# Kernel tuning notes

Measured on AMD Instinct MI355X. Metric: run time of the kernel, lower is better.

Reference implementation:

```python
import jax, jax.numpy as jnp
import numpy as np

B, N, D, H = 8, 1024, 512, 512  # batch, nodes/graph, input dim, hidden/output dim
NEG_SLOPE = 0.2


def _gatv2_layer(x, src, dst, Wl, bl, Wr, br, a, bias, nseg):
    """PyG GATv2Conv (heads=1, add_self_loops=False, eval mode -> no dropout).
    message j->i: alpha_ij = softmax_i( a . leaky_relu(xl[j] + xr[i]) ); out[i] = sum_j alpha_ij * xl[j] + bias
    """
    xl = x @ Wl + bl              # [nseg, H] source transform
    xr = x @ Wr + br              # [nseg, H] target transform
    e = jax.nn.leaky_relu(xl[src] + xr[dst], NEG_SLOPE) @ a  # [E] raw scores
    m = jax.lax.stop_gradient(jax.ops.segment_max(e, dst, num_segments=nseg))
    ex = jnp.exp(e - m[dst])
    s = jax.ops.segment_sum(ex, dst, num_segments=nseg)
    alpha = ex / s[dst]                                       # segment softmax over incoming edges
    out = jax.ops.segment_sum(alpha[:, None] * xl[src], dst, num_segments=nseg)
    return out + bias


def setup_inputs() -> dict:
    key = jax.random.key(0)
    rng = np.random.RandomState(0)
    # random per-graph adjacency, avg degree ~16; block-diagonal edge extraction
    adj_np = (rng.rand(B, N, N) < (16.0 / N))
    srcs, dsts = [], []
    for b in range(B):  # matches torch.nonzero(big_adj).t(): row=src, col=dst
        r, c = np.nonzero(adj_np[b])
        srcs.append(r + b * N)
        dsts.append(c + b * N)
    edge_index = jnp.asarray(np.stack([np.concatenate(srcs), np.concatenate(dsts)]).astype(np.int32))

    ks = jax.random.split(key, 32)
    def lin(k, fi, fo):
        return (jax.random.normal(k, (fi, fo), jnp.float32) / np.sqrt(fi)).astype(jnp.float32)
    inp = {
        "batch_graph": jax.random.normal(ks[0], (B, N, D), jnp.float32),
        "adj": jnp.asarray(adj_np.astype(np.float32)),
        "edge_index": edge_index,
    }
    dims = [(D, H), (H, H), (H, H)]
    for i, (fi, fo) in enumerate(dims, start=1):
        k = jax.random.split(ks[i], 6)
        inp[f"Wl{i}"] = lin(k[0], fi, fo)
        inp[f"bl{i}"] = jnp.zeros((fo,), jnp.float32)
        inp[f"Wr{i}"] = lin(k[1], fi, fo)
        inp[f"br{i}"] = jnp.zeros((fo,), jnp.float32)
        inp[f"a{i}"] = (jax.random.normal(k[2], (fo,), jnp.float32) / np.sqrt(fo)).astype(jnp.float32)
        inp[f"bias{i}"] = jnp.zeros((fo,), jnp.float32)
    return inp


def reference(batch_graph, adj, edge_index,
              Wl1, bl1, Wr1, br1, a1, bias1,
              Wl2, bl2, Wr2, br2, a2, bias2,
              Wl3, bl3, Wr3, br3, a3, bias3):
    b, n, d = batch_graph.shape
    nseg = b * n
    x = batch_graph.reshape(nseg, d)
    src, dst = edge_index[0], edge_index[1]
    x = _gatv2_layer(x, src, dst, Wl1, bl1, Wr1, br1, a1, bias1, nseg)  # graph_norm = Identity
    x = _gatv2_layer(x, src, dst, Wl2, bl2, Wr2, br2, a2, bias2, nseg)
    x = _gatv2_layer(x, src, dst, Wl3, bl3, Wr3, br3, a3, bias3, nseg)
    return x.reshape(b, n, -1)
```

## Files before the change

### kernel.cpp

```cpp
#include <hip/hip_runtime.h>
#include <math.h>

#define MTOT 8192
#define HD   512
#define NEG  0.2f

typedef __attribute__((ext_vector_type(8))) short bf16x8;
typedef __attribute__((ext_vector_type(4))) float floatx4;

__device__ inline unsigned short f2bf(float f) {
    unsigned int u = __float_as_uint(f);
    unsigned int r = (u + 0x7FFFu + ((u >> 16) & 1u)) >> 16;
    return (unsigned short)r;
}
__device__ inline float bf2f(unsigned short h) {
    return __uint_as_float(((unsigned int)h) << 16);
}


__global__ void count_deg(const int* __restrict__ dst, int* __restrict__ deg, int E) {
    int i = blockIdx.x * 256 + threadIdx.x;
    if (i < E) atomicAdd(&deg[dst[i]], 1);
}

__global__ __launch_bounds__(1024) void scan_offsets(const int* __restrict__ deg,
                                                     int* __restrict__ offs,
                                                     int* __restrict__ cursor) {
    __shared__ int part[1024];
    int tid = threadIdx.x;
    int base = tid * 8;
    int v[8]; int s = 0;
    #pragma unroll
    for (int i = 0; i < 8; ++i) { v[i] = deg[base + i]; s += v[i]; }
    part[tid] = s;
    __syncthreads();
    for (int off = 1; off < 1024; off <<= 1) {
        int t = (tid >= off) ? part[tid - off] : 0;
        __syncthreads();
        part[tid] += t;
        __syncthreads();
    }
    int run = (tid == 0) ? 0 : part[tid - 1];
    #pragma unroll
    for (int i = 0; i < 8; ++i) {
        offs[base + i] = run;
        cursor[base + i] = run;
        run += v[i];
    }
    if (tid == 1023) offs[MTOT] = run;
}

__global__ void scatter_edges(const int* __restrict__ src, const int* __restrict__ dst,
                              int* __restrict__ cursor, int* __restrict__ csr_src, int E) {
    int i = blockIdx.x * 256 + threadIdx.x;
    if (i < E) {
        int p = atomicAdd(&cursor[dst[i]], 1);
        csr_src[p] = src[i];
    }
}


__global__ __launch_bounds__(256) void prep_convert(
    const float* __restrict__ W0, const float* __restrict__ W1,
    const float* __restrict__ W2, const float* __restrict__ W3,
    const float* __restrict__ W4, const float* __restrict__ W5,
    unsigned short* __restrict__ wtbase,
    const float* __restrict__ X,
    unsigned short* __restrict__ Ahi, unsigned short* __restrict__ Alo,
    int* __restrict__ deg)
{
    int z = blockIdx.z;
    if (z == 7) {
        if (blockIdx.x == 0 && blockIdx.y == 0) {
            for (int i = threadIdx.x; i < MTOT; i += 256) deg[i] = 0;
        }
        return;
    }
    if (z == 6) {
        int bid = blockIdx.x * 16 + blockIdx.y;
        int t0 = bid * 256 + threadIdx.x;
        #pragma unroll
        for (int it = 0; it < 16; ++it) {
            int i = (t0 + it * 65536) * 4;
            float4 vv = *(const float4*)(X + i);
            ushort4 h, l;
            h.x = f2bf(vv.x); l.x = f2bf(vv.x - bf2f(h.x));
            h.y = f2bf(vv.y); l.y = f2bf(vv.y - bf2f(h.y));
            h.z = f2bf(vv.z); l.z = f2bf(vv.z - bf2f(h.z));
            h.w = f2bf(vv.w); l.w = f2bf(vv.w - bf2f(h.w));
            *(ushort4*)(Ahi + i) = h;
            *(ushort4*)(Alo + i) = l;
        }
        return;
    }
    const float* W = (z == 0) ? W0 : (z == 1) ? W1 : (z == 2) ? W2
                   : (z == 3) ? W3 : (z == 4) ? W4 : W5;
    int L = z >> 1, lr = z & 1;
    const size_t SZ = (size_t)HD * HD;
    unsigned short* Whi = wtbase + (L * 4 + lr * 2) * SZ;
    unsigned short* Wlo = Whi + SZ;

    __shared__ float t[32][33];
    int bx = blockIdx.x * 32;
    int by = blockIdx.y * 32;
    int tx = threadIdx.x & 31, ty = threadIdx.x >> 5;
    for (int i = ty; i < 32; i += 8)
        t[i][tx] = W[(size_t)(by + i) * HD + bx + tx];
    __syncthreads();
    for (int i = ty; i < 32; i += 8) {
        float vv = t[tx][i];
        unsigned short h = f2bf(vv);
        unsigned short l = f2bf(vv - bf2f(h));
        Whi[(size_t)(bx + i) * HD + by + tx] = h;
        Wlo[(size_t)(bx + i) * HD + by + tx] = l;
    }
}


__global__ __launch_bounds__(256) void gemm_mfma_dual(
    const unsigned short* __restrict__ Ahi, const unsigned short* __restrict__ Alo,
    const unsigned short* __restrict__ Bhi_l, const unsigned short* __restrict__ Blo_l,
    const unsigned short* __restrict__ Bhi_r, const unsigned short* __restrict__ Blo_r,
    const float* __restrict__ bias_l, const float* __restrict__ bias_r,
    float* __restrict__ Cl, float* __restrict__ Cr)
{
    const unsigned short* Bhi = blockIdx.z ? Bhi_r : Bhi_l;
    const unsigned short* Blo = blockIdx.z ? Blo_r : Blo_l;
    const float* bias         = blockIdx.z ? bias_r : bias_l;
    float* C                  = blockIdx.z ? Cr : Cl;

    __shared__ __align__(16) unsigned short lds[4 * 128 * 32];

    int tid = threadIdx.x;
    int wave = tid >> 6, lane = tid & 63;
    int bm = blockIdx.y * 128, bn = blockIdx.x * 128;

    const unsigned short* gsrc[4] = {Ahi, Alo, Bhi, Blo};
    int rowbase[4] = {bm, bm, bn, bn};

    const unsigned short* gbase =
        gsrc[wave] + (size_t)(rowbase[wave] + (lane >> 2)) * 512 + (lane & 3) * 8;

    floatx4 acc[4][4] = {};

    int wm = wave & 1, wn = wave >> 1;
    int lr = lane & 15, lq = lane >> 4;

    for (int k0 = 0; k0 < 512; k0 += 32) {
        const unsigned short* g = gbase + k0;
        #pragma unroll
        for (int rg = 0; rg < 8; ++rg) {
            __builtin_amdgcn_global_load_lds(
                (const __attribute__((address_space(1))) unsigned int*)(g + (size_t)rg * 16 * 512),
                (__attribute__((address_space(3))) unsigned int*)(&lds[wave * 4096 + rg * 512]),
                16, 0, 0);
        }
        __syncthreads();

        bf16x8 ah[4], al[4], bh[4], bl_[4];
        #pragma unroll
        for (int i = 0; i < 4; ++i) {
            int mrow = wm * 64 + i * 16 + lr;
            ah[i]  = *(const bf16x8*)&lds[0 * 4096 + mrow * 32 + lq * 8];
            al[i]  = *(const bf16x8*)&lds[1 * 4096 + mrow * 32 + lq * 8];
            int nrow = wn * 64 + i * 16 + lr;
            bh[i]  = *(const bf16x8*)&lds[2 * 4096 + nrow * 32 + lq * 8];
            bl_[i] = *(const bf16x8*)&lds[3 * 4096 + nrow * 32 + lq * 8];
        }
        #pragma unroll
        for (int i = 0; i < 4; ++i)
            #pragma unroll
            for (int j = 0; j < 4; ++j) {
                acc[i][j] = __builtin_amdgcn_mfma_f32_16x16x32_bf16(ah[i], bh[j],  acc[i][j], 0, 0, 0);
                acc[i][j] = __builtin_amdgcn_mfma_f32_16x16x32_bf16(ah[i], bl_[j], acc[i][j], 0, 0, 0);
                acc[i][j] = __builtin_amdgcn_mfma_f32_16x16x32_bf16(al[i], bh[j],  acc[i][j], 0, 0, 0);
            }
        __syncthreads();
    }

    #pragma unroll
    for (int j = 0; j < 4; ++j) {
        int n = bn + wn * 64 + j * 16 + lr;
        float bv = bias[n];
        #pragma unroll
        for (int i = 0; i < 4; ++i) {
            int mbase = bm + wm * 64 + i * 16 + lq * 4;
            #pragma unroll
            for (int r = 0; r < 4; ++r)
                C[(size_t)(mbase + r) * 512 + n] = acc[i][j][r] + bv;
        }
    }
}


__global__ __launch_bounds__(512) void gat_fused2(
    const float* __restrict__ xl, const float* __restrict__ xr,
    const float* __restrict__ avec, const float* __restrict__ bias,
    const int* __restrict__ offs, const int* __restrict__ csr_src,
    float* __restrict__ out, unsigned short* __restrict__ Ohi,
    unsigned short* __restrict__ Olo, int write_fp32)
{
    __shared__ float xr_sh[4][512];
    __shared__ float sc_sh[4][128];
    __shared__ float inv_sh[4];

    int gid = blockIdx.x;
    int nbase = ((gid & 7) << 10) + ((gid >> 3) << 2);
    int tid = threadIdx.x;
    int wv = tid >> 6, lane = tid & 63;

    int o0 = offs[nbase], o1 = offs[nbase + 1], o2 = offs[nbase + 2];
    int o3 = offs[nbase + 3], o4 = offs[nbase + 4];

    {
        int row = tid >> 7, col = tid & 127;
        *(float4*)&xr_sh[row][col * 4] =
            *(const float4*)(xr + (size_t)(nbase + row) * HD + col * 4);
    }
    __syncthreads();

    {
        int sub = lane >> 4, flane = lane & 15;
        float4 av[8];
        #pragma unroll
        for (int i = 0; i < 8; ++i)
            av[i] = *(const float4*)(avec + i * 64 + flane * 4);

        for (int p0 = o0 + wv * 4; p0 < o4; p0 += 32) {
            int p = p0 + sub;
            bool valid = p < o4;
            int pc = valid ? p : o0;
            int nid = (pc >= o1) + (pc >= o2) + (pc >= o3);
            int nb = (nid == 0) ? o0 : (nid == 1) ? o1 : (nid == 2) ? o2 : o3;
            int local = pc - nb;
            int j = csr_src[pc];
            const float* xls = xl + (size_t)j * HD;
            float pe = 0.f;
            #pragma unroll
            for (int i = 0; i < 8; ++i) {
                float4 xv = *(const float4*)(xls + i * 64 + flane * 4);
                float4 rv = *(const float4*)&xr_sh[nid][i * 64 + flane * 4];
                float t;
                t = xv.x + rv.x; pe += av[i].x * (t > 0.f ? t : NEG * t);
                t = xv.y + rv.y; pe += av[i].y * (t > 0.f ? t : NEG * t);
                t = xv.z + rv.z; pe += av[i].z * (t > 0.f ? t : NEG * t);
                t = xv.w + rv.w; pe += av[i].w * (t > 0.f ? t : NEG * t);
            }
            pe += __shfl_xor(pe, 1, 64);
            pe += __shfl_xor(pe, 2, 64);
            pe += __shfl_xor(pe, 4, 64);
            pe += __shfl_xor(pe, 8, 64);
            if (valid && flane == 0 && local < 128) sc_sh[nid][local] = pe;
        }
    }
    __syncthreads();

    if (wv < 4) {
        int nb  = (wv == 0) ? o0 : (wv == 1) ? o1 : (wv == 2) ? o2 : o3;
        int ne  = (wv == 0) ? o1 : (wv == 1) ? o2 : (wv == 2) ? o3 : o4;
        int dg = ne - nb; if (dg > 128) dg = 128;
        float s0v = (lane < dg) ? sc_sh[wv][lane] : -1e30f;
        float s1v = (lane + 64 < dg) ? sc_sh[wv][lane + 64] : -1e30f;
        float m = fmaxf(s0v, s1v);
        #pragma unroll
        for (int off = 32; off; off >>= 1) m = fmaxf(m, __shfl_xor(m, off, 64));
        float e0 = (lane < dg) ? __expf(s0v - m) : 0.f;
        float e1 = (lane + 64 < dg) ? __expf(s1v - m) : 0.f;
        if (lane < dg) sc_sh[wv][lane] = e0;
        if (lane + 64 < dg) sc_sh[wv][lane + 64] = e1;
        float s = e0 + e1;
        #pragma unroll
        for (int off = 32; off; off >>= 1) s += __shfl_xor(s, off, 64);
        if (lane == 0) inv_sh[wv] = (s > 0.f) ? 1.f / s : 0.f;
    }
    __syncthreads();

    int nid = wv & 3, half = wv >> 2;
    int node = nbase + nid;
    int nb  = (nid == 0) ? o0 : (nid == 1) ? o1 : (nid == 2) ? o2 : o3;
    int ne  = (nid == 0) ? o1 : (nid == 1) ? o2 : (nid == 2) ? o3 : o4;
    int dg = ne - nb; if (dg > 128) dg = 128;
    int hb = half * 256 + lane * 4;

    float4 acc = {0.f, 0.f, 0.f, 0.f};
    int p = 0;
    for (; p + 8 <= dg; p += 8) {
        float w[8]; const float* q[8];
        #pragma unroll
        for (int u = 0; u < 8; ++u) {
            w[u] = sc_sh[nid][p + u];
            q[u] = xl + (size_t)csr_src[nb + p + u] * HD + hb;
        }
        float4 x[8];
        #pragma unroll
        for (int u = 0; u < 8; ++u) x[u] = *(const float4*)q[u];
        #pragma unroll
        for (int u = 0; u < 8; ++u) {
            acc.x += w[u] * x[u].x; acc.y += w[u] * x[u].y;
            acc.z += w[u] * x[u].z; acc.w += w[u] * x[u].w;
        }
    }
    for (; p < dg; ++p) {
        float w = sc_sh[nid][p];
        const float* q = xl + (size_t)csr_src[nb + p] * HD + hb;
        float4 x = *(const float4*)q;
        acc.x += w * x.x; acc.y += w * x.y; acc.z += w * x.z; acc.w += w * x.w;
    }

    float inv = inv_sh[nid];
    float4 bv = *(const float4*)(bias + hb);
    float4 o = {acc.x * inv + bv.x, acc.y * inv + bv.y,
                acc.z * inv + bv.z, acc.w * inv + bv.w};

    if (write_fp32) {
        *(float4*)(out + (size_t)node * HD + hb) = o;
    } else {
        size_t rb = (size_t)node * HD + hb;
        ushort4 h, lo;
        h.x = f2bf(o.x); lo.x = f2bf(o.x - bf2f(h.x));
        h.y = f2bf(o.y); lo.y = f2bf(o.y - bf2f(h.y));
        h.z = f2bf(o.z); lo.z = f2bf(o.z - bf2f(h.z));
        h.w = f2bf(o.w); lo.w = f2bf(o.w - bf2f(h.w));
        *(ushort4*)(Ohi + rb) = h;
        *(ushort4*)(Olo + rb) = lo;
    }
}


extern "C" void kernel_launch(void* const* d_in, const int* in_sizes, int n_in,
                              void* d_out, int out_size, void* d_ws, size_t ws_size,
                              hipStream_t stream) {
    const float* x0 = (const float*)d_in[0];
    const int* eidx = (const int*)d_in[2];
    int E = in_sizes[2] / 2;
    const int* esrc = eidx;
    const int* edst = eidx + E;

    const float* Wl[3] = {(const float*)d_in[3],  (const float*)d_in[9],  (const float*)d_in[15]};
    const float* bl[3] = {(const float*)d_in[4],  (const float*)d_in[10], (const float*)d_in[16]};
    const float* Wr[3] = {(const float*)d_in[5],  (const float*)d_in[11], (const float*)d_in[17]};
    const float* br[3] = {(const float*)d_in[6],  (const float*)d_in[12], (const float*)d_in[18]};
    const float* av[3] = {(const float*)d_in[7],  (const float*)d_in[13], (const float*)d_in[19]};
    const float* bs[3] = {(const float*)d_in[8],  (const float*)d_in[14], (const float*)d_in[20]};

    char* w = (char*)d_ws;
    unsigned short* Ahi = (unsigned short*)w; w += (size_t)MTOT * HD * 2;
    unsigned short* Alo = (unsigned short*)w; w += (size_t)MTOT * HD * 2;
    unsigned short* wtbase = (unsigned short*)w; w += 12 * (size_t)HD * HD * 2;
    float* xl = (float*)w; w += (size_t)MTOT * HD * 4;
    float* xr = (float*)w; w += (size_t)MTOT * HD * 4;
    int* deg    = (int*)w;
    int* offs   = deg + MTOT;
    int* cursor = offs + MTOT + 8;
    int* csr    = cursor + MTOT;
    const size_t SZ = (size_t)HD * HD;

    prep_convert<<<dim3(16, 16, 8), 256, 0, stream>>>(
        Wl[0], Wr[0], Wl[1], Wr[1], Wl[2], Wr[2], wtbase, x0, Ahi, Alo, deg);

    count_deg<<<(E + 255) / 256, 256, 0, stream>>>(edst, deg, E);
    scan_offsets<<<1, 1024, 0, stream>>>(deg, offs, cursor);
    scatter_edges<<<(E + 255) / 256, 256, 0, stream>>>(esrc, edst, cursor, csr, E);

    dim3 ggrid(HD / 128, MTOT / 128, 2);
    for (int L = 0; L < 3; ++L) {
        gemm_mfma_dual<<<ggrid, 256, 0, stream>>>(Ahi, Alo,
            wtbase + (L * 4 + 0) * SZ, wtbase + (L * 4 + 1) * SZ,
            wtbase + (L * 4 + 2) * SZ, wtbase + (L * 4 + 3) * SZ,
            bl[L], br[L], xl, xr);
        int last = (L == 2);
        gat_fused2<<<MTOT / 4, 512, 0, stream>>>(xl, xr, av[L], bs[L], offs, csr,
                                                 last ? (float*)d_out : nullptr,
                                                 last ? nullptr : Ahi,
                                                 last ? nullptr : Alo,
                                                 last);
    }
}
```

Before: 350.9 us.

## Fuse whole GATv2 pipeline into one cooperative persistent kernel with grid syncs

```diff
diff --git a/kernel.cpp b/kernel.cpp
--- a/kernel.cpp
+++ b/kernel.cpp
@@ -1,5 +1,8 @@
 #include <hip/hip_runtime.h>
+#include <hip/hip_cooperative_groups.h>
 #include <math.h>
+
+namespace cg = cooperative_groups;
 
 #define MTOT 8192
 #define HD   512
@@ -15,6 +18,313 @@
 }
 __device__ inline float bf2f(unsigned short h) {
     return __uint_as_float(((unsigned int)h) << 16);
+}
+
+struct GParams {
+    const float* x0;
+    const int* esrc; const int* edst; int E;
+    const float* W6[6];
+    const float* bl[3]; const float* br[3];
+    const float* av[3]; const float* bs[3];
+    unsigned short* Ahi; unsigned short* Alo;
+    unsigned short* wtbase;
+    float* xl; float* xr;
+    int* deg; int* offs; int* cursor; int* csr;
+    float* out;
+};
+
+
+__global__ __launch_bounds__(512, 4) void gat_mega(GParams P) {
+    cg::grid_group grid = cg::this_grid();
+    __shared__ __align__(16) unsigned char smem[32768];
+    const size_t SZ = (size_t)HD * HD;
+
+    int bid = blockIdx.x;
+    int tid = threadIdx.x;
+    int wave = tid >> 6, lane = tid & 63;
+
+    {
+        int team = tid >> 8;
+        int ttid = tid & 255;
+        float (*tt)[33] = (float(*)[33])(smem + team * 4352);
+        int tx = ttid & 31, ty = ttid >> 5;
+        #pragma unroll
+        for (int r = 0; r < 2; ++r) {
+            int task = bid * 2 + team + r * 1024;
+            bool act = task < 1536;
+            int zm = act ? (task >> 8) : 0;
+            int tile = task & 255;
+            int bx = (tile & 15) * 32, by = (tile >> 4) * 32;
+            if (act) {
+                const float* W = P.W6[zm];
+                for (int i = ty; i < 32; i += 8)
+                    tt[i][tx] = W[(size_t)(by + i) * HD + bx + tx];
+            }
+            __syncthreads();
+            if (act) {
+                int L = zm >> 1, lr2 = zm & 1;
+                unsigned short* Whi = P.wtbase + (size_t)(L * 4 + lr2 * 2) * SZ;
+                unsigned short* Wlo = Whi + SZ;
+                for (int i = ty; i < 32; i += 8) {
+                    float vv = tt[tx][i];
+                    unsigned short h = f2bf(vv);
+                    unsigned short l = f2bf(vv - bf2f(h));
+                    Whi[(size_t)(bx + i) * HD + by + tx] = h;
+                    Wlo[(size_t)(bx + i) * HD + by + tx] = l;
+                }
+            }
+            __syncthreads();
+        }
+    }
+    {
+        int t0 = bid * 512 + tid;
+        #pragma unroll
+        for (int u = 0; u < 4; ++u) {
+            int i = (t0 + u * 262144) * 4;
+            float4 vv = *(const float4*)(P.x0 + i);
+            ushort4 h, l;
+            h.x = f2bf(vv.x); l.x = f2bf(vv.x - bf2f(h.x));
+            h.y = f2bf(vv.y); l.y = f2bf(vv.y - bf2f(h.y));
+            h.z = f2bf(vv.z); l.z = f2bf(vv.z - bf2f(h.z));
+            h.w = f2bf(vv.w); l.w = f2bf(vv.w - bf2f(h.w));
+            *(ushort4*)(P.Ahi + i) = h;
+            *(ushort4*)(P.Alo + i) = l;
+        }
+        if (t0 < MTOT) P.deg[t0] = 0;
+    }
+    grid.sync();
+
+    for (int i = bid * 512 + tid; i < P.E; i += 262144)
+        atomicAdd(&P.deg[P.edst[i]], 1);
+    grid.sync();
+
+    if (bid == 0) {
+        int* part = (int*)smem;
+        int base = tid * 16;
+        int v[16]; int s = 0;
+        #pragma unroll
+        for (int i = 0; i < 16; ++i) { v[i] = P.deg[base + i]; s += v[i]; }
+        part[tid] = s;
+        __syncthreads();
+        for (int off = 1; off < 512; off <<= 1) {
+            int t = (tid >= off) ? part[tid - off] : 0;
+            __syncthreads();
+            part[tid] += t;
+            __syncthreads();
+        }
+        int run = tid ? part[tid - 1] : 0;
+        #pragma unroll
+        for (int i = 0; i < 16; ++i) {
+            P.offs[base + i] = run;
+            P.cursor[base + i] = run;
+            run += v[i];
+        }
+        if (tid == 511) P.offs[MTOT] = run;
+    }
+    grid.sync();
+
+    for (int i = bid * 512 + tid; i < P.E; i += 262144) {
+        int d = P.edst[i];
+        int p = atomicAdd(&P.cursor[d], 1);
+        P.csr[p] = P.esrc[i];
+    }
+    grid.sync();
+
+    for (int L = 0; L < 3; ++L) {
+        {
+            unsigned short* lds = (unsigned short*)smem;
+            int z  = bid & 1;
+            int tn = (bid >> 1) & 3;
+            int tm = bid >> 3;
+            const unsigned short* Bhi = P.wtbase + (size_t)(L * 4 + z * 2) * SZ;
+            const unsigned short* Blo = Bhi + SZ;
+            const float* bias = z ? P.br[L] : P.bl[L];
+            float* C          = z ? P.xr : P.xl;
+            int bm = tm * 128, bn = tn * 128;
+
+            const unsigned short* gsrc4[4] = {P.Ahi, P.Alo, Bhi, Blo};
+            int rowb4[4] = {bm, bm, bn, bn};
+            int twv = wave >> 1, half = wave & 1;
+            const unsigned short* gbase =
+                gsrc4[twv] + (size_t)(rowb4[twv] + half * 64 + (lane >> 2)) * 512 + (lane & 3) * 8;
+
+            floatx4 acc[4][2] = {};
+            int wm2 = wave & 1, wn4 = wave >> 1;
+            int lr = lane & 15, lq = lane >> 4;
+
+            for (int k0 = 0; k0 < 512; k0 += 32) {
+                const unsigned short* g = gbase + k0;
+                #pragma unroll
+                for (int rg = 0; rg < 4; ++rg) {
+                    __builtin_amdgcn_global_load_lds(
+                        (const __attribute__((address_space(1))) unsigned int*)(g + (size_t)rg * 16 * 512),
+                        (__attribute__((address_space(3))) unsigned int*)(&lds[twv * 4096 + half * 2048 + rg * 512]),
+                        16, 0, 0);
+                }
+                __syncthreads();
+
+                bf16x8 ah[4], al[4], bh[2], bl_[2];
+                #pragma unroll
+                for (int i = 0; i < 4; ++i) {
+                    int mrow = wm2 * 64 + i * 16 + lr;
+                    ah[i] = *(const bf16x8*)&lds[0 * 4096 + mrow * 32 + lq * 8];
+                    al[i] = *(const bf16x8*)&lds[1 * 4096 + mrow * 32 + lq * 8];
+                }
+                #pragma unroll
+                for (int j = 0; j < 2; ++j) {
+                    int nrow = wn4 * 32 + j * 16 + lr;
+                    bh[j]  = *(const bf16x8*)&lds[2 * 4096 + nrow * 32 + lq * 8];
+                    bl_[j] = *(const bf16x8*)&lds[3 * 4096 + nrow * 32 + lq * 8];
+                }
+                #pragma unroll
+                for (int i = 0; i < 4; ++i)
+                    #pragma unroll
+                    for (int j = 0; j < 2; ++j) {
+                        acc[i][j] = __builtin_amdgcn_mfma_f32_16x16x32_bf16(ah[i], bh[j],  acc[i][j], 0, 0, 0);
+                        acc[i][j] = __builtin_amdgcn_mfma_f32_16x16x32_bf16(ah[i], bl_[j], acc[i][j], 0, 0, 0);
+                        acc[i][j] = __builtin_amdgcn_mfma_f32_16x16x32_bf16(al[i], bh[j],  acc[i][j], 0, 0, 0);
+                    }
+                __syncthreads();
+            }
+
+            #pragma unroll
+            for (int j = 0; j < 2; ++j) {
+                int n = bn + wn4 * 32 + j * 16 + lr;
+                float bv = bias[n];
+                #pragma unroll
+                for (int i = 0; i < 4; ++i) {
+                    int mb = bm + wm2 * 64 + i * 16 + lq * 4;
+                    #pragma unroll
+                    for (int r = 0; r < 4; ++r)
+                        C[(size_t)(mb + r) * 512 + n] = acc[i][j][r] + bv;
+                }
+            }
+        }
+        grid.sync();
+
+        {
+            int write_fp32 = (L == 2);
+            const float* avec = P.av[L];
+            const float* bias = P.bs[L];
+            float* sc = (float*)smem + wave * 128;
+            int nbase = ((bid & 7) << 10) + ((bid >> 3) << 4);
+
+            for (int nn = wave; nn < 16; nn += 8) {
+                int node = nbase + nn;
+                int beg = P.offs[node], end = P.offs[node + 1];
+                int dg = end - beg;
+                if (dg > 128) dg = 128;
+
+                {
+                    int sub = lane >> 4, flane = lane & 15;
+                    float4 avr[8], rv[8];
+                    const float* xrrow = P.xr + (size_t)node * HD;
+                    #pragma unroll
+                    for (int i = 0; i < 8; ++i) {
+                        avr[i] = *(const float4*)(avec + i * 64 + flane * 4);
+                        rv[i]  = *(const float4*)(xrrow + i * 64 + flane * 4);
+                    }
+                    for (int p0 = 0; p0 < dg; p0 += 4) {
+                        int p = p0 + sub;
+                        bool valid = p < dg;
+                        int j = P.csr[beg + (valid ? p : 0)];
+                        const float* xls = P.xl + (size_t)j * HD;
+                        float pe = 0.f;
+                        #pragma unroll
+                        for (int i = 0; i < 8; ++i) {
+                            float4 xv = *(const float4*)(xls + i * 64 + flane * 4);
+                            float t;
+                            t = xv.x + rv[i].x; pe += avr[i].x * (t > 0.f ? t : NEG * t);
+                            t = xv.y + rv[i].y; pe += avr[i].y * (t > 0.f ? t : NEG * t);
+                            t = xv.z + rv[i].z; pe += avr[i].z * (t > 0.f ? t : NEG * t);
+                            t = xv.w + rv[i].w; pe += avr[i].w * (t > 0.f ? t : NEG * t);
+                        }
+                        pe += __shfl_xor(pe, 1, 64);
+                        pe += __shfl_xor(pe, 2, 64);
+                        pe += __shfl_xor(pe, 4, 64);
+                        pe += __shfl_xor(pe, 8, 64);
+                        if (valid && flane == 0) sc[p] = pe;
+                    }
+                }
+
+                float s0v = (lane < dg) ? sc[lane] : -1e30f;
+                float s1v = (lane + 64 < dg) ? sc[lane + 64] : -1e30f;
+                float m = fmaxf(s0v, s1v);
+                #pragma unroll
+                for (int off = 32; off; off >>= 1) m = fmaxf(m, __shfl_xor(m, off, 64));
+                float e0 = (lane < dg) ? __expf(s0v - m) : 0.f;
+                float e1 = (lane + 64 < dg) ? __expf(s1v - m) : 0.f;
+                if (lane < dg) sc[lane] = e0;
+                if (lane + 64 < dg) sc[lane + 64] = e1;
+                float s = e0 + e1;
+                #pragma unroll
+                for (int off = 32; off; off >>= 1) s += __shfl_xor(s, off, 64);
+                float inv = (s > 0.f) ? 1.f / s : 0.f;
+
+                int h0 = lane << 2;
+                float4 acc0 = {0.f, 0.f, 0.f, 0.f}, acc1 = {0.f, 0.f, 0.f, 0.f};
+                int p = 0;
+                for (; p + 4 <= dg; p += 4) {
+                    float w0 = sc[p + 0], w1 = sc[p + 1], w2 = sc[p + 2], w3 = sc[p + 3];
+                    int j0 = P.csr[beg + p + 0], j1 = P.csr[beg + p + 1];
+                    int j2 = P.csr[beg + p + 2], j3 = P.csr[beg + p + 3];
+                    const float* q0 = P.xl + (size_t)j0 * HD;
+                    const float* q1 = P.xl + (size_t)j1 * HD;
+                    const float* q2 = P.xl + (size_t)j2 * HD;
+                    const float* q3 = P.xl + (size_t)j3 * HD;
+                    float4 x00 = *(const float4*)(q0 + h0), x01 = *(const float4*)(q0 + 256 + h0);
+                    float4 x10 = *(const float4*)(q1 + h0), x11 = *(const float4*)(q1 + 256 + h0);
+                    float4 x20 = *(const float4*)(q2 + h0), x21 = *(const float4*)(q2 + 256 + h0);
+                    float4 x30 = *(const float4*)(q3 + h0), x31 = *(const float4*)(q3 + 256 + h0);
+                    acc0.x += w0 * x00.x + w1 * x10.x + w2 * x20.x + w3 * x30.x;
+                    acc0.y += w0 * x00.y + w1 * x10.y + w2 * x20.y + w3 * x30.y;
+                    acc0.z += w0 * x00.z + w1 * x10.z + w2 * x20.z + w3 * x30.z;
+                    acc0.w += w0 * x00.w + w1 * x10.w + w2 * x20.w + w3 * x30.w;
+                    acc1.x += w0 * x01.x + w1 * x11.x + w2 * x21.x + w3 * x31.x;
+                    acc1.y += w0 * x01.y + w1 * x11.y + w2 * x21.y + w3 * x31.y;
+                    acc1.z += w0 * x01.z + w1 * x11.z + w2 * x21.z + w3 * x31.z;
+                    acc1.w += w0 * x01.w + w1 * x11.w + w2 * x21.w + w3 * x31.w;
+                }
+                for (; p < dg; ++p) {
+                    float w = sc[p];
+                    int j = P.csr[beg + p];
+                    const float* q = P.xl + (size_t)j * HD;
+                    float4 x0 = *(const float4*)(q + h0), x1 = *(const float4*)(q + 256 + h0);
+                    acc0.x += w * x0.x; acc0.y += w * x0.y; acc0.z += w * x0.z; acc0.w += w * x0.w;
+                    acc1.x += w * x1.x; acc1.y += w * x1.y; acc1.z += w * x1.z; acc1.w += w * x1.w;
+                }
+
+                float4 b0 = *(const float4*)(bias + h0);
+                float4 b1 = *(const float4*)(bias + 256 + h0);
+                float4 o0 = {acc0.x * inv + b0.x, acc0.y * inv + b0.y,
+                             acc0.z * inv + b0.z, acc0.w * inv + b0.w};
+                float4 o1 = {acc1.x * inv + b1.x, acc1.y * inv + b1.y,
+                             acc1.z * inv + b1.z, acc1.w * inv + b1.w};
+
+                if (write_fp32) {
+                    float* orow = P.out + (size_t)node * HD;
+                    *(float4*)(orow + h0) = o0;
+                    *(float4*)(orow + 256 + h0) = o1;
+                } else {
+                    size_t rb = (size_t)node * HD;
+                    ushort4 h, lo;
+                    h.x = f2bf(o0.x); lo.x = f2bf(o0.x - bf2f(h.x));
+                    h.y = f2bf(o0.y); lo.y = f2bf(o0.y - bf2f(h.y));
+                    h.z = f2bf(o0.z); lo.z = f2bf(o0.z - bf2f(h.z));
+                    h.w = f2bf(o0.w); lo.w = f2bf(o0.w - bf2f(h.w));
+                    *(ushort4*)(P.Ahi + rb + h0) = h;
+                    *(ushort4*)(P.Alo + rb + h0) = lo;
+                    h.x = f2bf(o1.x); lo.x = f2bf(o1.x - bf2f(h.x));
+                    h.y = f2bf(o1.y); lo.y = f2bf(o1.y - bf2f(h.y));
+                    h.z = f2bf(o1.z); lo.z = f2bf(o1.z - bf2f(h.z));
+                    h.w = f2bf(o1.w); lo.w = f2bf(o1.w - bf2f(h.w));
+                    *(ushort4*)(P.Ahi + rb + 256 + h0) = h;
+                    *(ushort4*)(P.Alo + rb + 256 + h0) = lo;
+                }
+            }
+        }
+        if (L < 2) grid.sync();
+    }
 }
 
 
@@ -59,7 +369,6 @@
     }
 }
 
-
 __global__ __launch_bounds__(256) void prep_convert(
     const float* __restrict__ W0, const float* __restrict__ W1,
     const float* __restrict__ W2, const float* __restrict__ W3,
@@ -116,7 +425,6 @@
     }
 }
 
-
 __global__ __launch_bounds__(256) void gemm_mfma_dual(
     const unsigned short* __restrict__ Ahi, const unsigned short* __restrict__ Alo,
     const unsigned short* __restrict__ Bhi_l, const unsigned short* __restrict__ Blo_l,
@@ -191,7 +499,6 @@
         }
     }
 }
-
 
 __global__ __launch_bounds__(512) void gat_fused2(
     const float* __restrict__ xl, const float* __restrict__ xr,
@@ -355,9 +662,25 @@
     int* csr    = cursor + MTOT;
     const size_t SZ = (size_t)HD * HD;
 
+    GParams P;
+    P.x0 = x0; P.esrc = esrc; P.edst = edst; P.E = E;
+    P.W6[0] = Wl[0]; P.W6[1] = Wr[0]; P.W6[2] = Wl[1];
+    P.W6[3] = Wr[1]; P.W6[4] = Wl[2]; P.W6[5] = Wr[2];
+    for (int i = 0; i < 3; ++i) {
+        P.bl[i] = bl[i]; P.br[i] = br[i]; P.av[i] = av[i]; P.bs[i] = bs[i];
+    }
+    P.Ahi = Ahi; P.Alo = Alo; P.wtbase = wtbase;
+    P.xl = xl; P.xr = xr;
+    P.deg = deg; P.offs = offs; P.cursor = cursor; P.csr = csr;
+    P.out = (float*)d_out;
+
+    void* args[] = {(void*)&P};
+    hipError_t err = hipLaunchCooperativeKernel((const void*)gat_mega,
+                                                dim3(512), dim3(512), args, 0, stream);
+    if (err == hipSuccess) return;
+
     prep_convert<<<dim3(16, 16, 8), 256, 0, stream>>>(
         Wl[0], Wr[0], Wl[1], Wr[1], Wl[2], Wr[2], wtbase, x0, Ahi, Alo, deg);
-
     count_deg<<<(E + 255) / 256, 256, 0, stream>>>(edst, deg, E);
     scan_offsets<<<1, 1024, 0, stream>>>(deg, offs, cursor);
     scatter_edges<<<(E + 255) / 256, 256, 0, stream>>>(esrc, edst, cursor, csr, E);
```

Result: slower. 989.1 us (+181.8%).

## Merge CSR prep into cooperative kernel and cache edge indices in LDS

Applied to the files above, without the earlier changes.

```diff
diff --git a/kernel.cpp b/kernel.cpp
--- a/kernel.cpp
+++ b/kernel.cpp
@@ -1,9 +1,11 @@
 #include <hip/hip_runtime.h>
+#include <hip/hip_cooperative_groups.h>
 #include <math.h>
+
+namespace cg = cooperative_groups;
 
 #define MTOT 8192
 #define HD   512
-#define NEG  0.2f
 
 typedef __attribute__((ext_vector_type(8))) short bf16x8;
 typedef __attribute__((ext_vector_type(4))) float floatx4;
@@ -15,6 +17,99 @@
 }
 __device__ inline float bf2f(unsigned short h) {
     return __uint_as_float(((unsigned int)h) << 16);
+}
+
+
+struct PrepParams {
+    const float* W6[6];
+    const float* x0;
+    unsigned short* wtbase;
+    unsigned short* Ahi; unsigned short* Alo;
+    const int* esrc; const int* edst; int E;
+    int* deg; int* offs; int* cursor; int* csr;
+};
+
+__global__ __launch_bounds__(256) void prep_csr(PrepParams P) {
+    cg::grid_group grid = cg::this_grid();
+    __shared__ float tt[32][33];
+    __shared__ int part[256];
+    int bid = blockIdx.x, tid = threadIdx.x;
+    const size_t SZ = (size_t)HD * HD;
+
+    #pragma unroll
+    for (int r = 0; r < 6; ++r) {
+        int task = bid + r * 256;
+        int zm = task >> 8;
+        int tile = task & 255;
+        int bx = (tile & 15) * 32, by = (tile >> 4) * 32;
+        const float* W = P.W6[zm];
+        int tx = tid & 31, ty = tid >> 5;
+        __syncthreads();
+        for (int i = ty; i < 32; i += 8)
+            tt[i][tx] = W[(size_t)(by + i) * HD + bx + tx];
+        __syncthreads();
+        int L = zm >> 1, lr2 = zm & 1;
+        unsigned short* Whi = P.wtbase + (size_t)(L * 4 + lr2 * 2) * SZ;
+        unsigned short* Wlo = Whi + SZ;
+        for (int i = ty; i < 32; i += 8) {
+            float vv = tt[tx][i];
+            unsigned short h = f2bf(vv);
+            unsigned short l = f2bf(vv - bf2f(h));
+            Whi[(size_t)(bx + i) * HD + by + tx] = h;
+            Wlo[(size_t)(bx + i) * HD + by + tx] = l;
+        }
+    }
+    {
+        int t0 = bid * 256 + tid;
+        #pragma unroll
+        for (int u = 0; u < 16; ++u) {
+            int i = (t0 + u * 65536) * 4;
+            float4 vv = *(const float4*)(P.x0 + i);
+            ushort4 h, l;
+            h.x = f2bf(vv.x); l.x = f2bf(vv.x - bf2f(h.x));
+            h.y = f2bf(vv.y); l.y = f2bf(vv.y - bf2f(h.y));
+            h.z = f2bf(vv.z); l.z = f2bf(vv.z - bf2f(h.z));
+            h.w = f2bf(vv.w); l.w = f2bf(vv.w - bf2f(h.w));
+            *(ushort4*)(P.Ahi + i) = h;
+            *(ushort4*)(P.Alo + i) = l;
+        }
+        if (t0 < MTOT) P.deg[t0] = 0;
+    }
+    grid.sync();
+
+    for (int i = bid * 256 + tid; i < P.E; i += 65536)
+        atomicAdd(&P.deg[P.edst[i]], 1);
+    grid.sync();
+
+    if (bid == 0) {
+        int base = tid * 32;
+        int v[32]; int s = 0;
+        #pragma unroll
+        for (int i = 0; i < 32; ++i) { v[i] = P.deg[base + i]; s += v[i]; }
+        part[tid] = s;
+        __syncthreads();
+        for (int off = 1; off < 256; off <<= 1) {
+            int t = (tid >= off) ? part[tid - off] : 0;
+            __syncthreads();
+            part[tid] += t;
+            __syncthreads();
+        }
+        int run = tid ? part[tid - 1] : 0;
+        #pragma unroll
+        for (int i = 0; i < 32; ++i) {
+            P.offs[base + i] = run;
+            P.cursor[base + i] = run;
+            run += v[i];
+        }
+        if (tid == 255) P.offs[MTOT] = run;
+    }
+    grid.sync();
+
+    for (int i = bid * 256 + tid; i < P.E; i += 65536) {
+        int d = P.edst[i];
+        int p = atomicAdd(&P.cursor[d], 1);
+        P.csr[p] = P.esrc[i];
+    }
 }
 
 
@@ -59,7 +154,6 @@
     }
 }
 
-
 __global__ __launch_bounds__(256) void prep_convert(
     const float* __restrict__ W0, const float* __restrict__ W1,
     const float* __restrict__ W2, const float* __restrict__ W3,
@@ -71,9 +165,8 @@
 {
     int z = blockIdx.z;
     if (z == 7) {
-        if (blockIdx.x == 0 && blockIdx.y == 0) {
+        if (blockIdx.x == 0 && blockIdx.y == 0)
             for (int i = threadIdx.x; i < MTOT; i += 256) deg[i] = 0;
-        }
         return;
     }
     if (z == 6) {
@@ -193,7 +286,7 @@
 }
 
 
-__global__ __launch_bounds__(512) void gat_fused2(
+__global__ __launch_bounds__(512) void gat_fused3(
     const float* __restrict__ xl, const float* __restrict__ xr,
     const float* __restrict__ avec, const float* __restrict__ bias,
     const int* __restrict__ offs, const int* __restrict__ csr_src,
@@ -202,6 +295,7 @@
 {
     __shared__ float xr_sh[4][512];
     __shared__ float sc_sh[4][128];
+    __shared__ int   idx_sh[4][128];
     __shared__ float inv_sh[4];
 
     int gid = blockIdx.x;
@@ -216,6 +310,12 @@
         int row = tid >> 7, col = tid & 127;
         *(float4*)&xr_sh[row][col * 4] =
             *(const float4*)(xr + (size_t)(nbase + row) * HD + col * 4);
+    }
+    if (wv < 4) {
+        int nb = (wv == 0) ? o0 : (wv == 1) ? o1 : (wv == 2) ? o2 : o3;
+        int ne = (wv == 0) ? o1 : (wv == 1) ? o2 : (wv == 2) ? o3 : o4;
+        int dg = ne - nb; if (dg > 128) dg = 128;
+        for (int i = lane; i < dg; i += 64) idx_sh[wv][i] = csr_src[nb + i];
     }
     __syncthreads();
 
@@ -233,31 +333,33 @@
             int nid = (pc >= o1) + (pc >= o2) + (pc >= o3);
             int nb = (nid == 0) ? o0 : (nid == 1) ? o1 : (nid == 2) ? o2 : o3;
             int local = pc - nb;
-            int j = csr_src[pc];
+            valid = valid && (local < 128);
+            int j = idx_sh[nid][valid ? local : 0];
             const float* xls = xl + (size_t)j * HD;
-            float pe = 0.f;
+            float pe0 = 0.f, pe1 = 0.f;
             #pragma unroll
             for (int i = 0; i < 8; ++i) {
                 float4 xv = *(const float4*)(xls + i * 64 + flane * 4);
                 float4 rv = *(const float4*)&xr_sh[nid][i * 64 + flane * 4];
                 float t;
-                t = xv.x + rv.x; pe += av[i].x * (t > 0.f ? t : NEG * t);
-                t = xv.y + rv.y; pe += av[i].y * (t > 0.f ? t : NEG * t);
-                t = xv.z + rv.z; pe += av[i].z * (t > 0.f ? t : NEG * t);
-                t = xv.w + rv.w; pe += av[i].w * (t > 0.f ? t : NEG * t);
+                t = xv.x + rv.x; pe0 = fmaf(av[i].x, t, pe0); pe1 = fmaf(av[i].x, fabsf(t), pe1);
+                t = xv.y + rv.y; pe0 = fmaf(av[i].y, t, pe0); pe1 = fmaf(av[i].y, fabsf(t), pe1);
+                t = xv.z + rv.z; pe0 = fmaf(av[i].z, t, pe0); pe1 = fmaf(av[i].z, fabsf(t), pe1);
+                t = xv.w + rv.w; pe0 = fmaf(av[i].w, t, pe0); pe1 = fmaf(av[i].w, fabsf(t), pe1);
             }
+            float pe = fmaf(0.6f, pe0, 0.4f * pe1);
             pe += __shfl_xor(pe, 1, 64);
             pe += __shfl_xor(pe, 2, 64);
             pe += __shfl_xor(pe, 4, 64);
             pe += __shfl_xor(pe, 8, 64);
-            if (valid && flane == 0 && local < 128) sc_sh[nid][local] = pe;
+            if (valid && flane == 0) sc_sh[nid][local] = pe;
         }
     }
     __syncthreads();
 
     if (wv < 4) {
-        int nb  = (wv == 0) ? o0 : (wv == 1) ? o1 : (wv == 2) ? o2 : o3;
-        int ne  = (wv == 0) ? o1 : (wv == 1) ? o2 : (wv == 2) ? o3 : o4;
+        int nb = (wv == 0) ? o0 : (wv == 1) ? o1 : (wv == 2) ? o2 : o3;
+        int ne = (wv == 0) ? o1 : (wv == 1) ? o2 : (wv == 2) ? o3 : o4;
         int dg = ne - nb; if (dg > 128) dg = 128;
         float s0v = (lane < dg) ? sc_sh[wv][lane] : -1e30f;
         float s1v = (lane + 64 < dg) ? sc_sh[wv][lane + 64] : -1e30f;
@@ -277,8 +379,8 @@
 
     int nid = wv & 3, half = wv >> 2;
     int node = nbase + nid;
-    int nb  = (nid == 0) ? o0 : (nid == 1) ? o1 : (nid == 2) ? o2 : o3;
-    int ne  = (nid == 0) ? o1 : (nid == 1) ? o2 : (nid == 2) ? o3 : o4;
+    int nb = (nid == 0) ? o0 : (nid == 1) ? o1 : (nid == 2) ? o2 : o3;
+    int ne = (nid == 0) ? o1 : (nid == 1) ? o2 : (nid == 2) ? o3 : o4;
     int dg = ne - nb; if (dg > 128) dg = 128;
     int hb = half * 256 + lane * 4;
 
@@ -289,7 +391,7 @@
         #pragma unroll
         for (int u = 0; u < 8; ++u) {
             w[u] = sc_sh[nid][p + u];
-            q[u] = xl + (size_t)csr_src[nb + p + u] * HD + hb;
+            q[u] = xl + (size_t)idx_sh[nid][p + u] * HD + hb;
         }
         float4 x[8];
         #pragma unroll
@@ -302,7 +404,7 @@
     }
     for (; p < dg; ++p) {
         float w = sc_sh[nid][p];
-        const float* q = xl + (size_t)csr_src[nb + p] * HD + hb;
+        const float* q = xl + (size_t)idx_sh[nid][p] * HD + hb;
         float4 x = *(const float4*)q;
         acc.x += w * x.x; acc.y += w * x.y; acc.z += w * x.z; acc.w += w * x.w;
     }
@@ -355,12 +457,23 @@
     int* csr    = cursor + MTOT;
     const size_t SZ = (size_t)HD * HD;
 
-    prep_convert<<<dim3(16, 16, 8), 256, 0, stream>>>(
-        Wl[0], Wr[0], Wl[1], Wr[1], Wl[2], Wr[2], wtbase, x0, Ahi, Alo, deg);
-
-    count_deg<<<(E + 255) / 256, 256, 0, stream>>>(edst, deg, E);
-    scan_offsets<<<1, 1024, 0, stream>>>(deg, offs, cursor);
-    scatter_edges<<<(E + 255) / 256, 256, 0, stream>>>(esrc, edst, cursor, csr, E);
+    PrepParams P;
+    P.W6[0] = Wl[0]; P.W6[1] = Wr[0]; P.W6[2] = Wl[1];
+    P.W6[3] = Wr[1]; P.W6[4] = Wl[2]; P.W6[5] = Wr[2];
+    P.x0 = x0; P.wtbase = wtbase; P.Ahi = Ahi; P.Alo = Alo;
+    P.esrc = esrc; P.edst = edst; P.E = E;
+    P.deg = deg; P.offs = offs; P.cursor = cursor; P.csr = csr;
+
+    void* args[] = {(void*)&P};
+    hipError_t err = hipLaunchCooperativeKernel((const void*)prep_csr,
+                                                dim3(256), dim3(256), args, 0, stream);
+    if (err != hipSuccess) {
+        prep_convert<<<dim3(16, 16, 8), 256, 0, stream>>>(
+            Wl[0], Wr[0], Wl[1], Wr[1], Wl[2], Wr[2], wtbase, x0, Ahi, Alo, deg);
+        count_deg<<<(E + 255) / 256, 256, 0, stream>>>(edst, deg, E);
+        scan_offsets<<<1, 1024, 0, stream>>>(deg, offs, cursor);
+        scatter_edges<<<(E + 255) / 256, 256, 0, stream>>>(esrc, edst, cursor, csr, E);
+    }
 
     dim3 ggrid(HD / 128, MTOT / 128, 2);
     for (int L = 0; L < 3; ++L) {
@@ -369,7 +482,7 @@
             wtbase + (L * 4 + 2) * SZ, wtbase + (L * 4 + 3) * SZ,
             bl[L], br[L], xl, xr);
         int last = (L == 2);
-        gat_fused2<<<MTOT / 4, 512, 0, stream>>>(xl, xr, av[L], bs[L], offs, csr,
+        gat_fused3<<<MTOT / 4, 512, 0, stream>>>(xl, xr, av[L], bs[L], offs, csr,
                                                  last ? (float*)d_out : nullptr,
                                                  last ? nullptr : Ahi,
                                                  last ? nullptr : Alo,
```

New measurement: 481.3 us. 1.37x slower.
